# Kernel optimization log

Hardware: AMD Instinct MI355X
Metric: run time of the kernel (lower is better)

## Reference

```python
import jax, jax.numpy as jnp
import numpy as np

B, N = 64, 4096          # batch of diagrams, points per diagram
H, W = 64, 64            # persistence-image resolution
L, R = 5, 256            # num_landscapes, landscape resolution
EPS = 1e-8


def setup_inputs() -> dict:
    key = jax.random.key(0)
    k1, = jax.random.split(key, 1)
    u = jax.random.uniform(k1, (B, N, 2), dtype=jnp.float32)
    birth = u[..., 0] * 0.5                      # births in [0, 0.5]
    death = birth + u[..., 1] * 0.5 + 1e-3       # deaths > births, in range
    pairs = jnp.stack([birth, death], axis=-1)   # (B, N, 2)
    sigma = jnp.float32(0.1)                     # learned bandwidth (nn.Parameter)
    return {"pairs": pairs, "sigma": sigma}


def reference(pairs, sigma):
    # ---- Persistence image (batched, vectorized over points) ----
    grid_x = jnp.linspace(0.0, 1.0, W, dtype=pairs.dtype)   # birth axis
    grid_y = jnp.linspace(0.0, 1.0, H, dtype=pairs.dtype)   # persistence axis
    birth = pairs[..., 0]                 # (B, N)
    death = pairs[..., 1]                 # (B, N)
    pers = death - birth                  # (B, N)
    # normalization per config ranges (0,1): divide by (range + 1e-8)
    birth_n = birth / (1.0 + EPS)
    pers_n = pers / (1.0 + EPS)
    weights = pers                        # weight_fn == 'linear'
    inv2s2 = 1.0 / (2.0 * sigma * sigma)
    # separable Gaussian factors: (B, N, W) and (B, N, H)
    gx = jnp.exp(-(grid_x[None, None, :] - birth_n[..., None]) ** 2 * inv2s2)
    gy = jnp.exp(-(grid_y[None, None, :] - pers_n[..., None]) ** 2 * inv2s2)
    # sum_n wt_n * gy_n(h) * gx_n(w)  ->  (B, H, W)
    image = jnp.einsum('bnh,bnw->bhw', gy * weights[..., None], gx)
    image = image / (jnp.max(image, axis=(1, 2), keepdims=True) + EPS)

    # ---- Persistence landscapes ----
    min_b = jnp.min(birth, axis=1, keepdims=True)   # (B, 1)
    max_d = jnp.max(death, axis=1, keepdims=True)   # (B, 1)
    frac = jnp.linspace(0.0, 1.0, R, dtype=pairs.dtype)
    t = min_b + (max_d - min_b) * frac[None, :]     # (B, R)
    rising = jnp.clip(t[:, None, :] - birth[..., None], 0.0)   # (B, N, R)
    falling = jnp.clip(death[..., None] - t[:, None, :], 0.0)  # (B, N, R)
    tents = jnp.minimum(rising, falling)                        # (B, N, R)
    # descending sort over points + take top L == top_k over point axis
    top = jax.lax.top_k(jnp.swapaxes(tents, 1, 2), L)[0]        # (B, R, L)
    landscapes = jnp.swapaxes(top, 1, 2)                        # (B, L, R)
    return image, landscapes
```

## Files before the change

kernel.cpp:

```cpp
#include <hip/hip_runtime.h>
#include <math.h>


#define B_   64
#define N_   4096
#define HW_  64
#define RES_ 256
#define EPSF 1e-8f
#define KC_  4
#define CPB  1024
#define KP   64
#define PCW  32
#define LCH  (N_ / PCW)

typedef short short8v  __attribute__((ext_vector_type(8)));
typedef float float4v  __attribute__((ext_vector_type(4)));

__device__ __forceinline__ unsigned short f2bf(float f) {
    unsigned int u = __float_as_uint(f);
    u += 0x7fffu + ((u >> 16) & 1u);
    return (unsigned short)(u >> 16);
}

#define INS5(v0, v1, v2, v3, v4, x)                       \
    {                                                     \
        float _p0 = v0, _p1 = v1, _p2 = v2, _p3 = v3;     \
        v0 = fmaxf(_p0, x);                               \
        v1 = __builtin_amdgcn_fmed3f(_p0, _p1, x);        \
        v2 = __builtin_amdgcn_fmed3f(_p1, _p2, x);        \
        v3 = __builtin_amdgcn_fmed3f(_p2, _p3, x);        \
        v4 = __builtin_amdgcn_fmed3f(_p3, v4, x);         \
    }

__global__ __launch_bounds__(256) void k_minmax(const float* __restrict__ pairs,
                                                float* __restrict__ wsf) {
    int b = blockIdx.x, tid = threadIdx.x;
    const float2* pr = (const float2*)pairs + (size_t)b * N_;
    float mn = 1e30f, mx = -1e30f;
    #pragma unroll
    for (int i = 0; i < N_ / 256; ++i) {
        float2 v = pr[tid + i * 256];
        mn = fminf(mn, v.x);
        mx = fmaxf(mx, v.y);
    }
    #pragma unroll
    for (int off = 32; off > 0; off >>= 1) {
        mn = fminf(mn, __shfl_xor(mn, off, 64));
        mx = fmaxf(mx, __shfl_xor(mx, off, 64));
    }
    __shared__ float smn[4], smx[4];
    if ((tid & 63) == 0) { smn[tid >> 6] = mn; smx[tid >> 6] = mx; }
    __syncthreads();
    if (tid == 0) {
        mn = fminf(fminf(smn[0], smn[1]), fminf(smn[2], smn[3]));
        mx = fmaxf(fmaxf(smx[0], smx[1]), fmaxf(smx[2], smx[3]));
        wsf[b]      = mn;
        wsf[64 + b] = mx;
    }
}

__global__ __launch_bounds__(256) void k_main(const float* __restrict__ pairs,
                                              const float* __restrict__ sigp,
                                              const float* __restrict__ wsf,
                                              float* __restrict__ part,
                                              float* __restrict__ lp) {
    __shared__ unsigned short gy_lds[64 * 72];
    __shared__ unsigned short gx_lds[64 * 72];
    __shared__ float2 pts_lds[CPB];

    int tid = threadIdx.x;
    int l = tid & 63, w = tid >> 6;

    if (blockIdx.x < 256) {
        int kc = blockIdx.x & 3, b = blockIdx.x >> 2;
        float sigma = sigp[0];
        float cc = 0.5f / (sigma * sigma);

        const float4* src = (const float4*)(pairs + 2 * ((size_t)b * N_ + kc * CPB));
        ((float4*)pts_lds)[tid]       = src[tid];
        ((float4*)pts_lds)[256 + tid] = src[256 + tid];

        int c  = tid & 63;
        int pg = tid >> 6;
        float xc = (float)c * (1.0f / 63.0f);

        float4v acc[4];
        #pragma unroll
        for (int c4 = 0; c4 < 4; ++c4) acc[c4] = (float4v){0.f, 0.f, 0.f, 0.f};

        int rowA = (w * 16 + (l & 15)) * 72 + (l >> 4) * 8;

        for (int ch = 0; ch < CPB / KP; ++ch) {
            __syncthreads();
            int p0 = ch * KP + pg * 16;
            alignas(16) unsigned short gyb[16], gxb[16];
            #pragma unroll
            for (int j = 0; j < 16; ++j) {
                float2 q = pts_lds[p0 + j];
                float pe = q.y - q.x;
                float dx = xc - q.x;
                float dy = xc - pe;
                gxb[j] = f2bf(__expf(-dx * dx * cc));
                gyb[j] = f2bf(pe * __expf(-dy * dy * cc));
            }
            *(uint4*)&gy_lds[c * 72 + pg * 16]     = *(uint4*)&gyb[0];
            *(uint4*)&gy_lds[c * 72 + pg * 16 + 8] = *(uint4*)&gyb[8];
            *(uint4*)&gx_lds[c * 72 + pg * 16]     = *(uint4*)&gxb[0];
            *(uint4*)&gx_lds[c * 72 + pg * 16 + 8] = *(uint4*)&gxb[8];
            __syncthreads();
            #pragma unroll
            for (int ks = 0; ks < 2; ++ks) {
                short8v af = *(const short8v*)&gy_lds[rowA + ks * 32];
                #pragma unroll
                for (int c4 = 0; c4 < 4; ++c4) {
                    short8v bf = *(const short8v*)
                        &gx_lds[(c4 * 16 + (l & 15)) * 72 + ks * 32 + (l >> 4) * 8];
                    acc[c4] = __builtin_amdgcn_mfma_f32_16x16x32_bf16(af, bf, acc[c4], 0, 0, 0);
                }
            }
        }

        float* dst = part + (size_t)(b * KC_ + kc) * (HW_ * HW_);
        #pragma unroll
        for (int c4 = 0; c4 < 4; ++c4)
            #pragma unroll
            for (int reg = 0; reg < 4; ++reg) {
                int h = w * 16 + (l >> 4) * 4 + reg;
                int wv = c4 * 16 + (l & 15);
                dst[h * HW_ + wv] = acc[c4][reg];
            }
    } else {
        int idx = blockIdx.x - 256;
        int b = idx >> 3, pcb = idx & 7;
        int pc = pcb * 4 + w;
        float minb = wsf[b], maxd = wsf[64 + b];
        float sc = (maxd - minb) * (1.0f / 255.0f);
        float t0 = minb + sc * (float)l;
        float t1 = t0 + sc * 64.0f;
        float t2 = t0 + sc * 128.0f;
        float t3 = t0 + sc * 192.0f;

        float a0 = 0.f, a1 = 0.f, a2 = 0.f, a3 = 0.f, a4 = 0.f;
        float b0 = 0.f, b1 = 0.f, b2 = 0.f, b3 = 0.f, b4 = 0.f;
        float c0 = 0.f, c1 = 0.f, c2 = 0.f, c3 = 0.f, c4 = 0.f;
        float d0 = 0.f, d1 = 0.f, d2 = 0.f, d3 = 0.f, d4 = 0.f;

        const float4* pw = (const float4*)(pairs + 2 * ((size_t)b * N_ + pc * LCH));
        #pragma unroll 4
        for (int p = 0; p < LCH / 2; ++p) {
            float4 q = pw[p];
            {
                float bb = q.x, dd = q.y;
                float x;
                x = fminf(t0 - bb, dd - t0); INS5(a0, a1, a2, a3, a4, x);
                x = fminf(t1 - bb, dd - t1); INS5(b0, b1, b2, b3, b4, x);
                x = fminf(t2 - bb, dd - t2); INS5(c0, c1, c2, c3, c4, x);
                x = fminf(t3 - bb, dd - t3); INS5(d0, d1, d2, d3, d4, x);
            }
            {
                float bb = q.z, dd = q.w;
                float x;
                x = fminf(t0 - bb, dd - t0); INS5(a0, a1, a2, a3, a4, x);
                x = fminf(t1 - bb, dd - t1); INS5(b0, b1, b2, b3, b4, x);
                x = fminf(t2 - bb, dd - t2); INS5(c0, c1, c2, c3, c4, x);
                x = fminf(t3 - bb, dd - t3); INS5(d0, d1, d2, d3, d4, x);
            }
        }

        float* dst = lp + (size_t)(b * PCW + pc) * 5 * RES_;
        dst[0*RES_ + l]       = a0; dst[1*RES_ + l]       = a1;
        dst[2*RES_ + l]       = a2; dst[3*RES_ + l]       = a3;
        dst[4*RES_ + l]       = a4;
        dst[0*RES_ + l + 64]  = b0; dst[1*RES_ + l + 64]  = b1;
        dst[2*RES_ + l + 64]  = b2; dst[3*RES_ + l + 64]  = b3;
        dst[4*RES_ + l + 64]  = b4;
        dst[0*RES_ + l + 128] = c0; dst[1*RES_ + l + 128] = c1;
        dst[2*RES_ + l + 128] = c2; dst[3*RES_ + l + 128] = c3;
        dst[4*RES_ + l + 128] = c4;
        dst[0*RES_ + l + 192] = d0; dst[1*RES_ + l + 192] = d1;
        dst[2*RES_ + l + 192] = d2; dst[3*RES_ + l + 192] = d3;
        dst[4*RES_ + l + 192] = d4;
    }
}

__global__ __launch_bounds__(256) void k_finish(const float* __restrict__ part,
                                                const float* __restrict__ lp,
                                                float* __restrict__ out) {
    int b = blockIdx.x, tid = threadIdx.x;

    const float4* p0 = (const float4*)(part + (size_t)b * KC_ * (HW_ * HW_));
    float4 s[4];
    float m = 0.0f;
    #pragma unroll
    for (int i = 0; i < 4; ++i) {
        int pix4 = tid + i * 256;
        float4 v = p0[pix4];
        #pragma unroll
        for (int kc = 1; kc < KC_; ++kc) {
            float4 u = p0[(size_t)kc * 1024 + pix4];
            v.x += u.x; v.y += u.y; v.z += u.z; v.w += u.w;
        }
        s[i] = v;
        m = fmaxf(m, fmaxf(fmaxf(v.x, v.y), fmaxf(v.z, v.w)));
    }
    #pragma unroll
    for (int off = 32; off > 0; off >>= 1) m = fmaxf(m, __shfl_xor(m, off, 64));
    __shared__ float sm[4];
    if ((tid & 63) == 0) sm[tid >> 6] = m;
    __syncthreads();
    m = fmaxf(fmaxf(sm[0], sm[1]), fmaxf(sm[2], sm[3]));
    float inv = 1.0f / (m + EPSF);
    float4* od = (float4*)(out + (size_t)b * (HW_ * HW_));
    #pragma unroll
    for (int i = 0; i < 4; ++i) {
        float4 v = s[i];
        v.x *= inv; v.y *= inv; v.z *= inv; v.w *= inv;
        od[tid + i * 256] = v;
    }

    float v0 = 0.f, v1 = 0.f, v2 = 0.f, v3 = 0.f, v4 = 0.f;
    const float* lpb = lp + (size_t)b * PCW * 5 * RES_;
    for (int pc = 0; pc < PCW; ++pc) {
        #pragma unroll
        for (int lvl = 0; lvl < 5; ++lvl) {
            float x = lpb[(pc * 5 + lvl) * RES_ + tid];
            INS5(v0, v1, v2, v3, v4, x);
        }
    }
    float* o = out + (size_t)B_ * HW_ * HW_ + (size_t)b * (5 * RES_);
    o[tid]            = v0;
    o[RES_ + tid]     = v1;
    o[2 * RES_ + tid] = v2;
    o[3 * RES_ + tid] = v3;
    o[4 * RES_ + tid] = v4;
}

extern "C" void kernel_launch(void* const* d_in, const int* in_sizes, int n_in,
                              void* d_out, int out_size, void* d_ws, size_t ws_size,
                              hipStream_t stream) {
    const float* pairs = (const float*)d_in[0];
    const float* sig   = (const float*)d_in[1];
    float* out = (float*)d_out;
    float* wsf = (float*)d_ws;

    float* part = wsf + 128;
    float* lp   = part + (size_t)B_ * KC_ * HW_ * HW_;

    k_minmax<<<B_, 256, 0, stream>>>(pairs, wsf);
    k_main<<<768, 256, 0, stream>>>(pairs, sig, wsf, part, lp);
    k_finish<<<B_, 256, 0, stream>>>(part, lp, out);
}
```

Baseline: 93.85 us.

## Fuse min/max and finish kernels into main kernel via last-block atomic reduction

Removes the separate min/max and finish launches. Each landscape block now computes the batch's min birth and max death itself, merges its four waves' top-5 lists in shared memory, and writes one partial per block. The last block per batch, found with an atomic counter, does the final image normalisation or landscape merge. This cuts launch overhead and inter-kernel gaps, at the cost of a memset, redundant min/max reads per block and serialized tail work in the last block.

Result: slower. 102.5 us (+9.2%).

```diff
diff --git a/kernel.cpp b/kernel.cpp
--- a/kernel.cpp
+++ b/kernel.cpp
@@ -10,8 +10,8 @@
 #define KC_  4
 #define CPB  1024
 #define KP   64
-#define PCW  32
-#define LCH  (N_ / PCW)
+#define LPB_ 8
+#define LCH  128
 
 typedef short short8v  __attribute__((ext_vector_type(8)));
 typedef float float4v  __attribute__((ext_vector_type(4)));
@@ -32,41 +32,27 @@
         v4 = __builtin_amdgcn_fmed3f(_p3, v4, x);         \
     }
 
-__global__ __launch_bounds__(256) void k_minmax(const float* __restrict__ pairs,
-                                                float* __restrict__ wsf) {
-    int b = blockIdx.x, tid = threadIdx.x;
-    const float2* pr = (const float2*)pairs + (size_t)b * N_;
-    float mn = 1e30f, mx = -1e30f;
-    #pragma unroll
-    for (int i = 0; i < N_ / 256; ++i) {
-        float2 v = pr[tid + i * 256];
-        mn = fminf(mn, v.x);
-        mx = fmaxf(mx, v.y);
-    }
-    #pragma unroll
-    for (int off = 32; off > 0; off >>= 1) {
-        mn = fminf(mn, __shfl_xor(mn, off, 64));
-        mx = fmaxf(mx, __shfl_xor(mx, off, 64));
-    }
-    __shared__ float smn[4], smx[4];
-    if ((tid & 63) == 0) { smn[tid >> 6] = mn; smx[tid >> 6] = mx; }
-    __syncthreads();
-    if (tid == 0) {
-        mn = fminf(fminf(smn[0], smn[1]), fminf(smn[2], smn[3]));
-        mx = fmaxf(fmaxf(smx[0], smx[1]), fmaxf(smx[2], smx[3]));
-        wsf[b]      = mn;
-        wsf[64 + b] = mx;
-    }
-}
+union SmemU {
+    struct {
+        unsigned short gy[64 * 72];
+        unsigned short gx[64 * 72];
+        float2 pts[CPB];
+    } img;
+    struct {
+        float lmerge[4 * 5 * RES_];
+        float red[8];
+    } land;
+};
 
 __global__ __launch_bounds__(256) void k_main(const float* __restrict__ pairs,
                                               const float* __restrict__ sigp,
-                                              const float* __restrict__ wsf,
                                               float* __restrict__ part,
-                                              float* __restrict__ lp) {
-    __shared__ unsigned short gy_lds[64 * 72];
-    __shared__ unsigned short gx_lds[64 * 72];
-    __shared__ float2 pts_lds[CPB];
+                                              float* __restrict__ lp,
+                                              int* __restrict__ ctr,
+                                              float* __restrict__ out) {
+    __shared__ SmemU sm;
+    __shared__ int last_flag;
+    __shared__ float redf[4];
 
     int tid = threadIdx.x;
     int l = tid & 63, w = tid >> 6;
@@ -77,8 +63,8 @@
         float cc = 0.5f / (sigma * sigma);
 
         const float4* src = (const float4*)(pairs + 2 * ((size_t)b * N_ + kc * CPB));
-        ((float4*)pts_lds)[tid]       = src[tid];
-        ((float4*)pts_lds)[256 + tid] = src[256 + tid];
+        ((float4*)sm.img.pts)[tid]       = src[tid];
+        ((float4*)sm.img.pts)[256 + tid] = src[256 + tid];
 
         int c  = tid & 63;
         int pg = tid >> 6;
@@ -96,25 +82,25 @@
             alignas(16) unsigned short gyb[16], gxb[16];
             #pragma unroll
             for (int j = 0; j < 16; ++j) {
-                float2 q = pts_lds[p0 + j];
+                float2 q = sm.img.pts[p0 + j];
                 float pe = q.y - q.x;
                 float dx = xc - q.x;
                 float dy = xc - pe;
                 gxb[j] = f2bf(__expf(-dx * dx * cc));
                 gyb[j] = f2bf(pe * __expf(-dy * dy * cc));
             }
-            *(uint4*)&gy_lds[c * 72 + pg * 16]     = *(uint4*)&gyb[0];
-            *(uint4*)&gy_lds[c * 72 + pg * 16 + 8] = *(uint4*)&gyb[8];
-            *(uint4*)&gx_lds[c * 72 + pg * 16]     = *(uint4*)&gxb[0];
-            *(uint4*)&gx_lds[c * 72 + pg * 16 + 8] = *(uint4*)&gxb[8];
+            *(uint4*)&sm.img.gy[c * 72 + pg * 16]     = *(uint4*)&gyb[0];
+            *(uint4*)&sm.img.gy[c * 72 + pg * 16 + 8] = *(uint4*)&gyb[8];
+            *(uint4*)&sm.img.gx[c * 72 + pg * 16]     = *(uint4*)&gxb[0];
+            *(uint4*)&sm.img.gx[c * 72 + pg * 16 + 8] = *(uint4*)&gxb[8];
             __syncthreads();
             #pragma unroll
             for (int ks = 0; ks < 2; ++ks) {
-                short8v af = *(const short8v*)&gy_lds[rowA + ks * 32];
+                short8v af = *(const short8v*)&sm.img.gy[rowA + ks * 32];
                 #pragma unroll
                 for (int c4 = 0; c4 < 4; ++c4) {
                     short8v bf = *(const short8v*)
-                        &gx_lds[(c4 * 16 + (l & 15)) * 72 + ks * 32 + (l >> 4) * 8];
+                        &sm.img.gx[(c4 * 16 + (l & 15)) * 72 + ks * 32 + (l >> 4) * 8];
                     acc[c4] = __builtin_amdgcn_mfma_f32_16x16x32_bf16(af, bf, acc[c4], 0, 0, 0);
                 }
             }
@@ -129,16 +115,74 @@
                 int wv = c4 * 16 + (l & 15);
                 dst[h * HW_ + wv] = acc[c4][reg];
             }
+
+        __syncthreads();
+        if (tid == 0) {
+            int old = __hip_atomic_fetch_add(&ctr[b], 1, __ATOMIC_ACQ_REL,
+                                             __HIP_MEMORY_SCOPE_AGENT);
+            last_flag = (old == KC_ - 1);
+        }
+        __syncthreads();
+        if (last_flag) {
+            const float4* p0 = (const float4*)(part + (size_t)b * KC_ * (HW_ * HW_));
+            float4 s[4];
+            float m = 0.0f;
+            #pragma unroll
+            for (int i = 0; i < 4; ++i) {
+                int pix4 = tid + i * 256;
+                float4 v = p0[pix4];
+                #pragma unroll
+                for (int k2 = 1; k2 < KC_; ++k2) {
+                    float4 u = p0[(size_t)k2 * 1024 + pix4];
+                    v.x += u.x; v.y += u.y; v.z += u.z; v.w += u.w;
+                }
+                s[i] = v;
+                m = fmaxf(m, fmaxf(fmaxf(v.x, v.y), fmaxf(v.z, v.w)));
+            }
+            #pragma unroll
+            for (int off = 32; off > 0; off >>= 1) m = fmaxf(m, __shfl_xor(m, off, 64));
+            if ((tid & 63) == 0) redf[tid >> 6] = m;
+            __syncthreads();
+            m = fmaxf(fmaxf(redf[0], redf[1]), fmaxf(redf[2], redf[3]));
+            float inv = 1.0f / (m + EPSF);
+            float4* od = (float4*)(out + (size_t)b * (HW_ * HW_));
+            #pragma unroll
+            for (int i = 0; i < 4; ++i) {
+                float4 v = s[i];
+                v.x *= inv; v.y *= inv; v.z *= inv; v.w *= inv;
+                od[tid + i * 256] = v;
+            }
+        }
     } else {
         int idx = blockIdx.x - 256;
         int b = idx >> 3, pcb = idx & 7;
+
+        const float4* pb4 = (const float4*)(pairs + 2 * (size_t)b * N_);
+        float mn = 1e30f, mx = -1e30f;
+        #pragma unroll
+        for (int i = 0; i < 8; ++i) {
+            float4 q = pb4[tid + i * 256];
+            mn = fminf(mn, fminf(q.x, q.z));
+            mx = fmaxf(mx, fmaxf(q.y, q.w));
+        }
+        #pragma unroll
+        for (int off = 32; off > 0; off >>= 1) {
+            mn = fminf(mn, __shfl_xor(mn, off, 64));
+            mx = fmaxf(mx, __shfl_xor(mx, off, 64));
+        }
+        if ((tid & 63) == 0) { sm.land.red[w] = mn; sm.land.red[4 + w] = mx; }
+        __syncthreads();
+        float minb = fminf(fminf(sm.land.red[0], sm.land.red[1]),
+                           fminf(sm.land.red[2], sm.land.red[3]));
+        float maxd = fmaxf(fmaxf(sm.land.red[4], sm.land.red[5]),
+                           fmaxf(sm.land.red[6], sm.land.red[7]));
+
         int pc = pcb * 4 + w;
-        float minb = wsf[b], maxd = wsf[64 + b];
-        float sc = (maxd - minb) * (1.0f / 255.0f);
-        float t0 = minb + sc * (float)l;
-        float t1 = t0 + sc * 64.0f;
-        float t2 = t0 + sc * 128.0f;
-        float t3 = t0 + sc * 192.0f;
+        float scl = (maxd - minb) * (1.0f / 255.0f);
+        float t0 = minb + scl * (float)l;
+        float t1 = t0 + scl * 64.0f;
+        float t2 = t0 + scl * 128.0f;
+        float t3 = t0 + scl * 192.0f;
 
         float a0 = 0.f, a1 = 0.f, a2 = 0.f, a3 = 0.f, a4 = 0.f;
         float b0 = 0.f, b1 = 0.f, b2 = 0.f, b3 = 0.f, b4 = 0.f;
@@ -167,72 +211,62 @@
             }
         }
 
-        float* dst = lp + (size_t)(b * PCW + pc) * 5 * RES_;
-        dst[0*RES_ + l]       = a0; dst[1*RES_ + l]       = a1;
-        dst[2*RES_ + l]       = a2; dst[3*RES_ + l]       = a3;
-        dst[4*RES_ + l]       = a4;
-        dst[0*RES_ + l + 64]  = b0; dst[1*RES_ + l + 64]  = b1;
-        dst[2*RES_ + l + 64]  = b2; dst[3*RES_ + l + 64]  = b3;
-        dst[4*RES_ + l + 64]  = b4;
-        dst[0*RES_ + l + 128] = c0; dst[1*RES_ + l + 128] = c1;
-        dst[2*RES_ + l + 128] = c2; dst[3*RES_ + l + 128] = c3;
-        dst[4*RES_ + l + 128] = c4;
-        dst[0*RES_ + l + 192] = d0; dst[1*RES_ + l + 192] = d1;
-        dst[2*RES_ + l + 192] = d2; dst[3*RES_ + l + 192] = d3;
-        dst[4*RES_ + l + 192] = d4;
+        __syncthreads();
+        float* lm = sm.land.lmerge;
+        lm[(w * 5 + 0) * RES_ + l]       = a0; lm[(w * 5 + 1) * RES_ + l]       = a1;
+        lm[(w * 5 + 2) * RES_ + l]       = a2; lm[(w * 5 + 3) * RES_ + l]       = a3;
+        lm[(w * 5 + 4) * RES_ + l]       = a4;
+        lm[(w * 5 + 0) * RES_ + l + 64]  = b0; lm[(w * 5 + 1) * RES_ + l + 64]  = b1;
+        lm[(w * 5 + 2) * RES_ + l + 64]  = b2; lm[(w * 5 + 3) * RES_ + l + 64]  = b3;
+        lm[(w * 5 + 4) * RES_ + l + 64]  = b4;
+        lm[(w * 5 + 0) * RES_ + l + 128] = c0; lm[(w * 5 + 1) * RES_ + l + 128] = c1;
+        lm[(w * 5 + 2) * RES_ + l + 128] = c2; lm[(w * 5 + 3) * RES_ + l + 128] = c3;
+        lm[(w * 5 + 4) * RES_ + l + 128] = c4;
+        lm[(w * 5 + 0) * RES_ + l + 192] = d0; lm[(w * 5 + 1) * RES_ + l + 192] = d1;
+        lm[(w * 5 + 2) * RES_ + l + 192] = d2; lm[(w * 5 + 3) * RES_ + l + 192] = d3;
+        lm[(w * 5 + 4) * RES_ + l + 192] = d4;
+        __syncthreads();
+
+        float v0 = lm[0 * RES_ + tid], v1 = lm[1 * RES_ + tid], v2 = lm[2 * RES_ + tid],
+              v3 = lm[3 * RES_ + tid], v4 = lm[4 * RES_ + tid];
+        #pragma unroll
+        for (int wv = 1; wv < 4; ++wv)
+            #pragma unroll
+            for (int lvl = 0; lvl < 5; ++lvl) {
+                float x = lm[(wv * 5 + lvl) * RES_ + tid];
+                INS5(v0, v1, v2, v3, v4, x);
+            }
+        float* dl = lp + (size_t)(b * LPB_ + pcb) * 5 * RES_;
+        dl[0 * RES_ + tid] = v0; dl[1 * RES_ + tid] = v1; dl[2 * RES_ + tid] = v2;
+        dl[3 * RES_ + tid] = v3; dl[4 * RES_ + tid] = v4;
+
+        __syncthreads();
+        if (tid == 0) {
+            int old = __hip_atomic_fetch_add(&ctr[64 + b], 1, __ATOMIC_ACQ_REL,
+                                             __HIP_MEMORY_SCOPE_AGENT);
+            last_flag = (old == LPB_ - 1);
+        }
+        __syncthreads();
+        if (last_flag) {
+            const float* lpb = lp + (size_t)b * LPB_ * 5 * RES_;
+            float u0 = lpb[0 * RES_ + tid], u1 = lpb[1 * RES_ + tid],
+                  u2 = lpb[2 * RES_ + tid], u3 = lpb[3 * RES_ + tid],
+                  u4 = lpb[4 * RES_ + tid];
+            for (int p2 = 1; p2 < LPB_; ++p2) {
+                #pragma unroll
+                for (int lvl = 0; lvl < 5; ++lvl) {
+                    float x = lpb[(p2 * 5 + lvl) * RES_ + tid];
+                    INS5(u0, u1, u2, u3, u4, x);
+                }
+            }
+            float* o = out + (size_t)B_ * HW_ * HW_ + (size_t)b * (5 * RES_);
+            o[tid]            = u0;
+            o[RES_ + tid]     = u1;
+            o[2 * RES_ + tid] = u2;
+            o[3 * RES_ + tid] = u3;
+            o[4 * RES_ + tid] = u4;
+        }
     }
-}
-
-__global__ __launch_bounds__(256) void k_finish(const float* __restrict__ part,
-                                                const float* __restrict__ lp,
-                                                float* __restrict__ out) {
-    int b = blockIdx.x, tid = threadIdx.x;
-
-    const float4* p0 = (const float4*)(part + (size_t)b * KC_ * (HW_ * HW_));
-    float4 s[4];
-    float m = 0.0f;
-    #pragma unroll
-    for (int i = 0; i < 4; ++i) {
-        int pix4 = tid + i * 256;
-        float4 v = p0[pix4];
-        #pragma unroll
-        for (int kc = 1; kc < KC_; ++kc) {
-            float4 u = p0[(size_t)kc * 1024 + pix4];
-            v.x += u.x; v.y += u.y; v.z += u.z; v.w += u.w;
-        }
-        s[i] = v;
-        m = fmaxf(m, fmaxf(fmaxf(v.x, v.y), fmaxf(v.z, v.w)));
-    }
-    #pragma unroll
-    for (int off = 32; off > 0; off >>= 1) m = fmaxf(m, __shfl_xor(m, off, 64));
-    __shared__ float sm[4];
-    if ((tid & 63) == 0) sm[tid >> 6] = m;
-    __syncthreads();
-    m = fmaxf(fmaxf(sm[0], sm[1]), fmaxf(sm[2], sm[3]));
-    float inv = 1.0f / (m + EPSF);
-    float4* od = (float4*)(out + (size_t)b * (HW_ * HW_));
-    #pragma unroll
-    for (int i = 0; i < 4; ++i) {
-        float4 v = s[i];
-        v.x *= inv; v.y *= inv; v.z *= inv; v.w *= inv;
-        od[tid + i * 256] = v;
-    }
-
-    float v0 = 0.f, v1 = 0.f, v2 = 0.f, v3 = 0.f, v4 = 0.f;
-    const float* lpb = lp + (size_t)b * PCW * 5 * RES_;
-    for (int pc = 0; pc < PCW; ++pc) {
-        #pragma unroll
-        for (int lvl = 0; lvl < 5; ++lvl) {
-            float x = lpb[(pc * 5 + lvl) * RES_ + tid];
-            INS5(v0, v1, v2, v3, v4, x);
-        }
-    }
-    float* o = out + (size_t)B_ * HW_ * HW_ + (size_t)b * (5 * RES_);
-    o[tid]            = v0;
-    o[RES_ + tid]     = v1;
-    o[2 * RES_ + tid] = v2;
-    o[3 * RES_ + tid] = v3;
-    o[4 * RES_ + tid] = v4;
 }
 
 extern "C" void kernel_launch(void* const* d_in, const int* in_sizes, int n_in,
@@ -243,10 +277,10 @@
     float* out = (float*)d_out;
     float* wsf = (float*)d_ws;
 
+    int*   ctr  = (int*)wsf;
     float* part = wsf + 128;
     float* lp   = part + (size_t)B_ * KC_ * HW_ * HW_;
 
-    k_minmax<<<B_, 256, 0, stream>>>(pairs, wsf);
-    k_main<<<768, 256, 0, stream>>>(pairs, sig, wsf, part, lp);
-    k_finish<<<B_, 256, 0, stream>>>(part, lp, out);
+    hipMemsetAsync(ctr, 0, 128 * sizeof(int), stream);
+    k_main<<<768, 256, 0, stream>>>(pairs, sig, part, lp, ctr, out);
 }
```
